# Kernel tuning notes

Hardware: AMD Instinct MI355X
Metric: run time of the kernel (lower is better)

Reference implementation:

```python
import jax, jax.numpy as jnp
import numpy as np
from jax import lax

BLANK = 27
NEG = -1e30  # safe -inf substitute (avoids NaN grads through logaddexp)


def _joint_log_probs(enc, dec, We, Wd, bf, Wp, bp):
    # Concat-then-Linear == sum of per-branch matmuls: [e;d] @ Wf = e@We + d@Wd.
    f = jnp.einsum('bte,eh->bth', enc, We)          # [B,T,H]
    g = jnp.einsum('bud,dh->buh', dec, Wd)          # [B,U1,H]
    h = jnp.tanh(f[:, :, None, :] + g[:, None, :, :] + bf)  # [B,T,U1,H]
    logits = jnp.einsum('btuh,hv->btuv', h, Wp) + bp         # [B,T,U1,V]
    return jax.nn.log_softmax(logits, axis=-1)


def _rnnt_loss_one(lp, tgt, t_len, u_len):
    # lp: [T,U1,V] log-probs, tgt: [U] int labels, t_len/u_len: scalars.
    T, U1, V = lp.shape
    blank_lp = lp[:, :, BLANK]                                   # [T,U1]
    lab_lp = jnp.take_along_axis(lp[:, :U1 - 1, :],
                                 tgt[None, :, None], axis=2)[..., 0]  # [T,U]

    # alpha[0,:] : only label emissions along u at t=0.
    alpha0 = jnp.concatenate([jnp.zeros((1,), lp.dtype),
                              jnp.cumsum(lab_lp[0])])            # [U1]

    def step(prev_alpha, inp):
        b_prev, lab_t = inp                       # [U1], [U]
        from_below = prev_alpha + b_prev          # blank move from t-1
        first = from_below[0]

        def inner(carry, x):
            fb, lab = x
            new = jnp.logaddexp(fb, carry + lab)  # blank-from-below vs label-from-left
            return new, new

        _, rest = lax.scan(inner, first, (from_below[1:], lab_t))
        alpha_t = jnp.concatenate([first[None], rest])
        return alpha_t, alpha_t

    _, alphas = lax.scan(step, alpha0, (blank_lp[:-1], lab_lp[1:]))
    alpha = jnp.concatenate([alpha0[None], alphas], axis=0)      # [T,U1]

    # Terminal: emit final blank at (t_len-1, u_len).
    return -(alpha[t_len - 1, u_len] + blank_lp[t_len - 1, u_len])


def setup_inputs() -> dict:
    key = jax.random.key(0)
    ks = jax.random.split(key, 10)
    B, T, U, E, D, H, V = 8, 400, 60, 256, 256, 512, 28
    enc_state = jax.random.normal(ks[0], (B, T, E), jnp.float32)
    dec_state = jax.random.normal(ks[1], (B, U + 1, D), jnp.float32)
    targets = jax.random.randint(ks[2], (B, U), 0, BLANK, jnp.int32)
    inputs_length = jax.random.randint(ks[3], (B,), 200, T + 1, jnp.int32)
    targets_length = jax.random.randint(ks[4], (B,), 30, U + 1, jnp.int32)
    s1 = 1.0 / np.sqrt(E + D)
    s2 = 1.0 / np.sqrt(H)
    We = jax.random.normal(ks[5], (E, H), jnp.float32) * s1
    Wd = jax.random.normal(ks[6], (D, H), jnp.float32) * s1
    bf = jax.random.normal(ks[7], (H,), jnp.float32) * s1
    Wp = jax.random.normal(ks[8], (H, V), jnp.float32) * s2
    bp = jax.random.normal(ks[9], (V,), jnp.float32) * s2
    return {"enc_state": enc_state, "dec_state": dec_state,
            "We": We, "Wd": Wd, "bf": bf, "Wp": Wp, "bp": bp,
            "targets": targets, "inputs_length": inputs_length,
            "targets_length": targets_length}


def reference(enc_state, dec_state, We, Wd, bf, Wp, bp,
              targets, inputs_length, targets_length):
    lp = _joint_log_probs(enc_state, dec_state, We, Wd, bf, Wp, bp)
    loss = jax.vmap(_rnnt_loss_one)(lp, targets, inputs_length, targets_length)
    return loss  # [B], reduction='none'
```

## Files before the change

kernel.cpp:

```cpp
#include <hip/hip_runtime.h>
#include <hip/hip_bf16.h>
#include <math.h>

#define NEGF (-1e30f)
#define LOG2E 1.4426950408889634f
#define LN2F 0.6931471805599453f
#define TSCALE 2.885390081777927f

typedef __attribute__((ext_vector_type(8))) short bf16x8;
typedef __attribute__((ext_vector_type(4))) float f32x4;

#define DROWS_PAD 480
#define DPITCH 64
#define CH 48

__device__ __forceinline__ unsigned short f2bf(float x) {
    __hip_bfloat16 h = __float2bfloat16(x);
    return *reinterpret_cast<unsigned short*>(&h);
}

__device__ __forceinline__ float wave_shr1(float x) {
    int i = __builtin_bit_cast(int, x);
    int r = __builtin_amdgcn_update_dpp(0, i, 0x138, 0xf, 0xf, true);
    return __builtin_bit_cast(float, r);
}

__device__ __forceinline__ float4 rcp4_nr(float4 d) {
    float4 y;
    y.x = __builtin_bit_cast(float, 0x7EF311C3 - __builtin_bit_cast(int, d.x));
    y.y = __builtin_bit_cast(float, 0x7EF311C3 - __builtin_bit_cast(int, d.y));
    y.z = __builtin_bit_cast(float, 0x7EF311C3 - __builtin_bit_cast(int, d.z));
    y.w = __builtin_bit_cast(float, 0x7EF311C3 - __builtin_bit_cast(int, d.w));
    float4 t;
    t.x = fmaf(-d.x, y.x, 2.f); t.y = fmaf(-d.y, y.y, 2.f);
    t.z = fmaf(-d.z, y.z, 2.f); t.w = fmaf(-d.w, y.w, 2.f);
    y.x *= t.x; y.y *= t.y; y.z *= t.z; y.w *= t.w;
    return y;
}

__global__ __launch_bounds__(256) void k_pack(const float* __restrict__ We,
                                              const float* __restrict__ Wd,
                                              const float* __restrict__ Wp,
                                              const float* __restrict__ bp,
                                              unsigned short* __restrict__ WeFrag,
                                              unsigned short* __restrict__ WdFrag,
                                              unsigned short* __restrict__ BfragP,
                                              float* __restrict__ csbp) {
    int gid = blockIdx.x * 256 + threadIdx.x;
    if (gid < 32768) {
        const float* W = (gid < 16384) ? We : Wd;
        unsigned short* F = (gid < 16384) ? WeFrag : WdFrag;
        int s = gid & 16383;
        int lane = s & 63;
        int c = (s >> 6) & 7;
        int nt = s >> 9;
        int n = nt * 16 + (lane & 15);
        int kbase = c * 32 + ((lane >> 4) & 3) * 8;
        unsigned short* dst = F + (size_t)s * 8;
#pragma unroll
        for (int j = 0; j < 8; ++j) dst[j] = f2bf(W[(size_t)(kbase + j) * 512 + n]);
    } else if (gid < 34816) {
        int s = gid - 32768;
        int lane = s & 63;
        int half = (s >> 6) & 1;
        int c = s >> 7;
        int n = half * 16 + (lane & 15);
        int kbase = c * 32 + (lane >> 4) * 8;
        unsigned short* dst = BfragP + (size_t)s * 8;
#pragma unroll
        for (int j = 0; j < 8; ++j) {
            float v = (n < 28) ? (-2.f * Wp[(kbase + j) * 28 + n]) : 0.f;
            dst[j] = f2bf(v);
        }
    } else if (gid < 34848) {
        int v = gid - 34816;
        float s = 0.f;
        if (v < 28) {
            for (int k = 0; k < 512; ++k) s += Wp[k * 28 + v];
            s += bp[v];
        }
        csbp[v] = s;
    }
}

__global__ __launch_bounds__(256) void k_gemm(const float* __restrict__ enc,
                                              const float* __restrict__ dec,
                                              const float* __restrict__ bfv,
                                              const unsigned short* __restrict__ WeFrag,
                                              const unsigned short* __restrict__ WdFrag,
                                              float* __restrict__ f,
                                              float* __restrict__ g) {
    const int wid = blockIdx.x * 4 + threadIdx.y;
    const int lane = threadIdx.x;
    const int m16 = lane & 15;
    const int quad = lane >> 4;

    const float* A; const unsigned short* WF; float* Out; int M, rt, ct; bool isg;
    if (wid < 1600) { A = enc; WF = WeFrag; Out = f; M = 3200; rt = wid >> 3; ct = wid & 7; isg = false; }
    else { int w2 = wid - 1600; A = dec; WF = WdFrag; Out = g; M = 488; rt = w2 >> 3; ct = w2 & 7; isg = true; }

    const int row = rt * 16 + m16;
    const float* arow = A + (size_t)min(row, M - 1) * 256 + quad * 8;

    f32x4 acc[4];
#pragma unroll
    for (int i = 0; i < 4; ++i) acc[i] = (f32x4){0.f, 0.f, 0.f, 0.f};

#pragma unroll
    for (int c = 0; c < 8; ++c) {
        float4 a0 = *(const float4*)(arow + c * 32);
        float4 a1 = *(const float4*)(arow + c * 32 + 4);
        union { unsigned short s[8]; bf16x8 v; } Af;
        Af.s[0] = f2bf(a0.x); Af.s[1] = f2bf(a0.y);
        Af.s[2] = f2bf(a0.z); Af.s[3] = f2bf(a0.w);
        Af.s[4] = f2bf(a1.x); Af.s[5] = f2bf(a1.y);
        Af.s[6] = f2bf(a1.z); Af.s[7] = f2bf(a1.w);
#pragma unroll
        for (int i = 0; i < 4; ++i) {
            int nt = ct * 4 + i;
            bf16x8 Bv = *(const bf16x8*)(WF + (size_t)((nt * 8 + c) * 64 + lane) * 8);
            acc[i] = __builtin_amdgcn_mfma_f32_16x16x32_bf16(Af.v, Bv, acc[i], 0, 0, 0);
        }
    }

#pragma unroll
    for (int i = 0; i < 4; ++i) {
        int n = ct * 64 + i * 16 + m16;
        float bv = isg ? bfv[n] : 0.f;
#pragma unroll
        for (int r = 0; r < 4; ++r) {
            int ro = rt * 16 + quad * 4 + r;
            if (ro < M) Out[(size_t)ro * 512 + n] = (acc[i][r] + bv) * TSCALE;
        }
    }
}

__global__ __launch_bounds__(512, 4) void k_cells(const float* __restrict__ f,
                                                  const float* __restrict__ g,
                                                  const unsigned short* __restrict__ Bfrag,
                                                  const float* __restrict__ csbp,
                                                  const int* __restrict__ targets,
                                                  const int* __restrict__ ilen,
                                                  const int* __restrict__ ulenp,
                                                  float2* __restrict__ pairD) {
    const int b = blockIdx.z;
    const int tlen = ilen[b];
    const int ulen = ulenp[b];
    const int t0 = blockIdx.x * 16;
    if (t0 >= tlen) return;
    if ((int)blockIdx.y * 8 > ulen) return;
    const int wave = threadIdx.y;
    const int lane = threadIdx.x;
    const int tid = wave * 64 + lane;

    __shared__ float fs[16 * 516];

    {
        const float4* src = (const float4*)(f + (size_t)(b * 400 + t0) * 512);
#pragma unroll
        for (int i = 0; i < 4; ++i) {
            int idx = tid + i * 512;
            int row = idx >> 7;
            int c4 = idx & 127;
            float4 v = src[idx];
            *(float4*)&fs[row * 516 + c4 * 4] = v;
        }
    }
    __syncthreads();

    const int quad = lane >> 4;
    const int m16 = lane & 15;
    const int u_raw = blockIdx.y * 8 + wave;
    const int u = min(u_raw, 60);
    const float* fsrow = fs + m16 * 516 + quad * 8;
    const float* gu = g + (size_t)(b * 61 + u) * 512 + quad * 8;
    const float4 one4 = make_float4(1.f, 1.f, 1.f, 1.f);

    f32x4 acc0 = {0.f, 0.f, 0.f, 0.f};
    f32x4 acc1 = {0.f, 0.f, 0.f, 0.f};

    float4 FA[2], FB[2], GA[2], GB[2];
    bf16x8 BR0[2], BR1[2];
#pragma unroll
    for (int c0 = 0; c0 < 2; ++c0) {
        FA[c0] = *(const float4*)(fsrow + c0 * 32);
        FB[c0] = *(const float4*)(fsrow + c0 * 32 + 4);
        GA[c0] = *(const float4*)(gu + c0 * 32);
        GB[c0] = *(const float4*)(gu + c0 * 32 + 4);
        BR0[c0] = *(const bf16x8*)(Bfrag + ((size_t)((c0 * 2 + 0) * 64 + lane)) * 8);
        BR1[c0] = *(const bf16x8*)(Bfrag + ((size_t)((c0 * 2 + 1) * 64 + lane)) * 8);
    }

#pragma unroll
    for (int c = 0; c < 16; ++c) {
        const int cu = c & 1;
        float4 fa = FA[cu], fb = FB[cu], ga = GA[cu], gb = GB[cu];
        bf16x8 b0 = BR0[cu], b1 = BR1[cu];
        if (c < 14) {
            FA[cu] = *(const float4*)(fsrow + (c + 2) * 32);
            FB[cu] = *(const float4*)(fsrow + (c + 2) * 32 + 4);
            GA[cu] = *(const float4*)(gu + (c + 2) * 32);
            GB[cu] = *(const float4*)(gu + (c + 2) * 32 + 4);
            BR0[cu] = *(const bf16x8*)(Bfrag + ((size_t)(((c + 2) * 2 + 0) * 64 + lane)) * 8);
            BR1[cu] = *(const bf16x8*)(Bfrag + ((size_t)(((c + 2) * 2 + 1) * 64 + lane)) * 8);
        }
        float4 s0 = fa + ga;
        float4 s1 = fb + gb;
        float4 e0, e1;
        e0.x = __builtin_amdgcn_exp2f(s0.x); e0.y = __builtin_amdgcn_exp2f(s0.y);
        e0.z = __builtin_amdgcn_exp2f(s0.z); e0.w = __builtin_amdgcn_exp2f(s0.w);
        e1.x = __builtin_amdgcn_exp2f(s1.x); e1.y = __builtin_amdgcn_exp2f(s1.y);
        e1.z = __builtin_amdgcn_exp2f(s1.z); e1.w = __builtin_amdgcn_exp2f(s1.w);
        float4 r0 = rcp4_nr(e0 + one4);
        float4 r1 = rcp4_nr(e1 + one4);
        union { unsigned short s[8]; bf16x8 v; } A;
        A.s[0] = f2bf(r0.x); A.s[1] = f2bf(r0.y);
        A.s[2] = f2bf(r0.z); A.s[3] = f2bf(r0.w);
        A.s[4] = f2bf(r1.x); A.s[5] = f2bf(r1.y);
        A.s[6] = f2bf(r1.z); A.s[7] = f2bf(r1.w);
        acc0 = __builtin_amdgcn_mfma_f32_16x16x32_bf16(A.v, b0, acc0, 0, 0, 0);
        acc1 = __builtin_amdgcn_mfma_f32_16x16x32_bf16(A.v, b1, acc1, 0, 0, 0);
    }

    const float cs0 = csbp[m16];
    const int n1 = 16 + m16;
    const bool n1v = (n1 < 28);
    const float cs1 = csbp[n1 & 31];
    int tv = targets[b * 60 + min(u, 59)];

    float res_blank[4], res_lab[4];
#pragma unroll
    for (int r = 0; r < 4; ++r) {
        float l0 = acc0[r] + cs0;
        float l1 = n1v ? (acc1[r] + cs1) : NEGF;
        float mx = fmaxf(l0, l1);
        mx = fmaxf(mx, __shfl_xor(mx, 1, 64));
        mx = fmaxf(mx, __shfl_xor(mx, 2, 64));
        mx = fmaxf(mx, __shfl_xor(mx, 4, 64));
        mx = fmaxf(mx, __shfl_xor(mx, 8, 64));
        float s = __builtin_amdgcn_exp2f((l0 - mx) * LOG2E) +
                  __builtin_amdgcn_exp2f((l1 - mx) * LOG2E);
        s += __shfl_xor(s, 1, 64);
        s += __shfl_xor(s, 2, 64);
        s += __shfl_xor(s, 4, 64);
        s += __shfl_xor(s, 8, 64);
        float lse = mx + __logf(s);
        int base = lane & 48;
        float labsrc = (tv < 16) ? l0 : l1;
        float labv = __shfl(labsrc, base | (tv & 15), 64);
        float blankv = __shfl(l1, base | 11, 64);
        res_blank[r] = (blankv - lse) * LOG2E;
        res_lab[r] = (labv - lse) * LOG2E;
    }

    if (m16 == 0 && u_raw <= 60) {
        float2* Pd = pairD + (size_t)b * (DROWS_PAD * DPITCH);
#pragma unroll
        for (int r = 0; r < 4; ++r) {
            int t = t0 + quad * 4 + r;
            if (t < tlen) {
                int d = t + u;
                float2 pr;
                pr.x = res_blank[r];
                pr.y = (u <= 59) ? res_lab[r] : NEGF;
                Pd[d * DPITCH + u] = pr;
            }
        }
    }
}

__global__ __launch_bounds__(256) void k_alpha(const float2* __restrict__ pairD,
                                               const int* __restrict__ ilen,
                                               const int* __restrict__ ulenp,
                                               float* __restrict__ out) {
    const int b = blockIdx.x;
    const int u = threadIdx.x;
    const int w = threadIdx.y;
    const float2* Pd = pairD + (size_t)b * (DROWS_PAD * DPITCH);
    const int tl = ilen[b];
    const int ul = ulenp[b];
    const int dstar = tl - 1 + ul;
    const int NCH = (dstar + CH - 1) / CH;
    const bool uok = (u <= 60);
    const bool lok = (u >= 1 && u <= 60);

    __shared__ char lbuf[2 * CH * 512];

    {
        const int tid = w * 64 + u;
        const float4* gs = (const float4*)Pd;
        float4* ld = (float4*)lbuf;
#pragma unroll
        for (int j = 0; j < 6; ++j) ld[tid + j * 256] = gs[tid + j * 256];
    }
    __syncthreads();

    float cur = (u == 0) ? 0.f : NEGF;
    float saved = NEGF, savedBlank = NEGF;

    for (int k = 0; k < NCH; ++k) {
        if (w > 0 && (k + 1) < NCH) {
            const int pt = (w - 1) * 64 + u;
            const float4* gs = (const float4*)(Pd + (size_t)(k + 1) * CH * DPITCH);
            float4* ld = (float4*)(lbuf + ((k + 1) & 1) * (CH * 512));
#pragma unroll
            for (int j = 0; j < 8; ++j)
                ld[pt + j * 192] = gs[pt + j * 192];
        }
        if (w == 0) {
            const char* base = lbuf + (k & 1) * (CH * 512);
            const int d0 = k * CH + 1;
#pragma unroll 16
            for (int r = 0; r < CH; ++r) {
                const int d = d0 + r;
                float2 v = *(const float2*)(base + r * 512 + u * 8);
                int t = d - u;
                float bv = (t >= 1 && t <= 399 && uok) ? v.x : NEGF;
                float lvn = wave_shr1(v.y);
                float lv = (lok && t >= 0 && t <= 399) ? lvn : NEGF;
                float up = wave_shr1(cur);
                float a = cur + bv;
                float c2 = up + lv;
                float mx = fmaxf(a, c2), mn = fminf(a, c2);
                float nv = mx + __log2f(1.f + __builtin_amdgcn_exp2f(mn - mx));
                bool valid = (t >= 0 && t <= 399 && uok);
                cur = valid ? nv : cur;
                saved = (d == dstar) ? cur : saved;
                savedBlank = (d == dstar) ? v.x : savedBlank;
            }
        }
        __syncthreads();
    }
    if (w == 0 && u == ul) out[b] = -(saved + savedBlank) * LN2F;
}

extern "C" void kernel_launch(void* const* d_in, const int* in_sizes, int n_in,
                              void* d_out, int out_size, void* d_ws, size_t ws_size,
                              hipStream_t stream) {
    const float* enc = (const float*)d_in[0];
    const float* dec = (const float*)d_in[1];
    const float* We  = (const float*)d_in[2];
    const float* Wd  = (const float*)d_in[3];
    const float* bf  = (const float*)d_in[4];
    const float* Wp  = (const float*)d_in[5];
    const float* bp  = (const float*)d_in[6];
    const int* targets = (const int*)d_in[7];
    const int* ilen    = (const int*)d_in[8];
    const int* ulen    = (const int*)d_in[9];
    float* out = (float*)d_out;
    float* ws = (float*)d_ws;

    float* f     = ws;
    float* g     = ws + 1638400;
    unsigned short* BfragP = (unsigned short*)(ws + 1888256);
    unsigned short* WeFrag = (unsigned short*)(ws + 1896448);
    unsigned short* WdFrag = (unsigned short*)(ws + 1961984);
    float* csbp  = ws + 2027520;
    float2* pairD = (float2*)(ws + 2027552);

    k_pack<<<137, 256, 0, stream>>>(We, Wd, Wp, bp, WeFrag, WdFrag, BfragP, csbp);

    k_gemm<<<462, dim3(64, 4, 1), 0, stream>>>(enc, dec, bf, WeFrag, WdFrag, f, g);

    dim3 gridC(25, 8, 8);
    dim3 blockC(64, 8, 1);
    k_cells<<<gridC, blockC, 0, stream>>>(f, g, BfragP, csbp, targets, ilen, ulen, pairD);

    k_alpha<<<8, dim3(64, 4, 1), 0, stream>>>(pairD, ilen, ulen, out);
}
```

Measured before the change: 142.9 us.

## Fuse alpha recursion into cells kernel with per-chunk completion counters

Removes the separate alpha launch and runs the alpha recursion in eight extra blocks of the cells kernel, one per batch element. These blocks poll per-(batch, time-chunk) atomic counters that cell blocks bump when they finish, and start each diagonal chunk once the time chunks it needs are done. The aim is to overlap the serial alpha scan with cell production and to drop one kernel launch boundary. The cost is spinning blocks that hold CU slots, relaxed atomic stores and loads with no explicit fences, and a counter reset added to the pack kernel.

```diff
diff --git a/kernel.cpp b/kernel.cpp
--- a/kernel.cpp
+++ b/kernel.cpp
@@ -45,7 +45,8 @@
                                               unsigned short* __restrict__ WeFrag,
                                               unsigned short* __restrict__ WdFrag,
                                               unsigned short* __restrict__ BfragP,
-                                              float* __restrict__ csbp) {
+                                              float* __restrict__ csbp,
+                                              int* __restrict__ doneCnt) {
     int gid = blockIdx.x * 256 + threadIdx.x;
     if (gid < 32768) {
         const float* W = (gid < 16384) ? We : Wd;
@@ -80,6 +81,8 @@
             s += bp[v];
         }
         csbp[v] = s;
+    } else if (gid < 35104) {
+        doneCnt[gid - 34848] = 0;
     }
 }
 
@@ -142,7 +145,95 @@
                                                   const int* __restrict__ targets,
                                                   const int* __restrict__ ilen,
                                                   const int* __restrict__ ulenp,
-                                                  float2* __restrict__ pairD) {
+                                                  float2* __restrict__ pairD,
+                                                  int* __restrict__ doneCnt,
+                                                  float* __restrict__ out) {
+    __shared__ char smem[49152];
+
+    if (blockIdx.x == 25) {
+        if (blockIdx.z != 0) return;
+        const int w = threadIdx.y;
+        if (w >= 4) return;
+        const int b = blockIdx.y;
+        const int u = threadIdx.x;
+        const float2* Pd = pairD + (size_t)b * (DROWS_PAD * DPITCH);
+        const unsigned long long* Pq = (const unsigned long long*)Pd;
+        const int* dn = doneCnt + b * 32;
+        const int tl = ilen[b];
+        const int ul = ulenp[b];
+        const int dstar = tl - 1 + ul;
+        const int NCH = (dstar + CH - 1) / CH;
+        const int tcLast = (tl - 1) >> 4;
+        const int nU = (ul >> 3) + 1;
+        const bool uok = (u <= 60);
+        const bool lok = (u >= 1 && u <= 60);
+        unsigned long long* lq = (unsigned long long*)smem;
+
+        int tcCur = -1;
+        auto gate = [&](int need) {
+            need = min(need, tcLast);
+            int guard = 0;
+            while (tcCur < need) {
+                int c_ = __hip_atomic_load(dn + tcCur + 1, __ATOMIC_RELAXED,
+                                           __HIP_MEMORY_SCOPE_AGENT);
+                if (c_ >= nU) { ++tcCur; }
+                else { __builtin_amdgcn_s_sleep(2);
+                       if (++guard > (1 << 22)) break; }
+            }
+        };
+
+        gate(2);
+        {
+            const int tid = w * 64 + u;
+#pragma unroll
+            for (int j = 0; j < 12; ++j)
+                lq[tid + j * 256] = __hip_atomic_load(Pq + tid + j * 256,
+                                        __ATOMIC_RELAXED, __HIP_MEMORY_SCOPE_AGENT);
+        }
+        __syncthreads();
+
+        float cur = (u == 0) ? 0.f : NEGF;
+        float saved = NEGF, savedBlank = NEGF;
+
+        for (int k = 0; k < NCH; ++k) {
+            if (w > 0 && (k + 1) < NCH) {
+                gate(3 * (k + 1) + 2);
+                const int pt = (w - 1) * 64 + u;
+                const unsigned long long* gs = Pq + (size_t)(k + 1) * (CH * DPITCH);
+                unsigned long long* ld = lq + ((k + 1) & 1) * (CH * 64);
+#pragma unroll
+                for (int j = 0; j < 16; ++j)
+                    ld[pt + j * 192] = __hip_atomic_load(gs + pt + j * 192,
+                                           __ATOMIC_RELAXED, __HIP_MEMORY_SCOPE_AGENT);
+            }
+            if (w == 0) {
+                const unsigned long long* baseq = lq + (k & 1) * (CH * 64);
+                const int d0 = k * CH + 1;
+#pragma unroll 16
+                for (int r = 0; r < CH; ++r) {
+                    const int d = d0 + r;
+                    float2 v = __builtin_bit_cast(float2, baseq[r * 64 + u]);
+                    int t = d - u;
+                    float bv = (t >= 1 && t <= 399 && uok) ? v.x : NEGF;
+                    float lvn = wave_shr1(v.y);
+                    float lv = (lok && t >= 0 && t <= 399) ? lvn : NEGF;
+                    float up = wave_shr1(cur);
+                    float a = cur + bv;
+                    float c2 = up + lv;
+                    float mx = fmaxf(a, c2), mn = fminf(a, c2);
+                    float nv = mx + __log2f(1.f + __builtin_amdgcn_exp2f(mn - mx));
+                    bool valid = (t >= 0 && t <= 399 && uok);
+                    cur = valid ? nv : cur;
+                    saved = (d == dstar) ? cur : saved;
+                    savedBlank = (d == dstar) ? v.x : savedBlank;
+                }
+            }
+            __syncthreads();
+        }
+        if (w == 0 && u == ul) out[b] = -(saved + savedBlank) * LN2F;
+        return;
+    }
+
     const int b = blockIdx.z;
     const int tlen = ilen[b];
     const int ulen = ulenp[b];
@@ -152,8 +243,7 @@
     const int wave = threadIdx.y;
     const int lane = threadIdx.x;
     const int tid = wave * 64 + lane;
-
-    __shared__ float fs[16 * 516];
+    float* fs = (float*)smem;
 
     {
         const float4* src = (const float4*)(f + (size_t)(b * 400 + t0) * 512);
@@ -263,75 +353,18 @@
                 float2 pr;
                 pr.x = res_blank[r];
                 pr.y = (u <= 59) ? res_lab[r] : NEGF;
-                Pd[d * DPITCH + u] = pr;
+                __hip_atomic_store((unsigned long long*)&Pd[d * DPITCH + u],
+                                   __builtin_bit_cast(unsigned long long, pr),
+                                   __ATOMIC_RELAXED, __HIP_MEMORY_SCOPE_AGENT);
             }
         }
     }
-}
-
-__global__ __launch_bounds__(256) void k_alpha(const float2* __restrict__ pairD,
-                                               const int* __restrict__ ilen,
-                                               const int* __restrict__ ulenp,
-                                               float* __restrict__ out) {
-    const int b = blockIdx.x;
-    const int u = threadIdx.x;
-    const int w = threadIdx.y;
-    const float2* Pd = pairD + (size_t)b * (DROWS_PAD * DPITCH);
-    const int tl = ilen[b];
-    const int ul = ulenp[b];
-    const int dstar = tl - 1 + ul;
-    const int NCH = (dstar + CH - 1) / CH;
-    const bool uok = (u <= 60);
-    const bool lok = (u >= 1 && u <= 60);
-
-    __shared__ char lbuf[2 * CH * 512];
-
-    {
-        const int tid = w * 64 + u;
-        const float4* gs = (const float4*)Pd;
-        float4* ld = (float4*)lbuf;
-#pragma unroll
-        for (int j = 0; j < 6; ++j) ld[tid + j * 256] = gs[tid + j * 256];
-    }
+
     __syncthreads();
-
-    float cur = (u == 0) ? 0.f : NEGF;
-    float saved = NEGF, savedBlank = NEGF;
-
-    for (int k = 0; k < NCH; ++k) {
-        if (w > 0 && (k + 1) < NCH) {
-            const int pt = (w - 1) * 64 + u;
-            const float4* gs = (const float4*)(Pd + (size_t)(k + 1) * CH * DPITCH);
-            float4* ld = (float4*)(lbuf + ((k + 1) & 1) * (CH * 512));
-#pragma unroll
-            for (int j = 0; j < 8; ++j)
-                ld[pt + j * 192] = gs[pt + j * 192];
-        }
-        if (w == 0) {
-            const char* base = lbuf + (k & 1) * (CH * 512);
-            const int d0 = k * CH + 1;
-#pragma unroll 16
-            for (int r = 0; r < CH; ++r) {
-                const int d = d0 + r;
-                float2 v = *(const float2*)(base + r * 512 + u * 8);
-                int t = d - u;
-                float bv = (t >= 1 && t <= 399 && uok) ? v.x : NEGF;
-                float lvn = wave_shr1(v.y);
-                float lv = (lok && t >= 0 && t <= 399) ? lvn : NEGF;
-                float up = wave_shr1(cur);
-                float a = cur + bv;
-                float c2 = up + lv;
-                float mx = fmaxf(a, c2), mn = fminf(a, c2);
-                float nv = mx + __log2f(1.f + __builtin_amdgcn_exp2f(mn - mx));
-                bool valid = (t >= 0 && t <= 399 && uok);
-                cur = valid ? nv : cur;
-                saved = (d == dstar) ? cur : saved;
-                savedBlank = (d == dstar) ? v.x : savedBlank;
-            }
-        }
-        __syncthreads();
-    }
-    if (w == 0 && u == ul) out[b] = -(saved + savedBlank) * LN2F;
+    if (tid == 0) {
+        __hip_atomic_fetch_add(doneCnt + b * 32 + blockIdx.x, 1,
+                               __ATOMIC_RELAXED, __HIP_MEMORY_SCOPE_AGENT);
+    }
 }
 
 extern "C" void kernel_launch(void* const* d_in, const int* in_sizes, int n_in,
@@ -357,14 +390,14 @@
     unsigned short* WdFrag = (unsigned short*)(ws + 1961984);
     float* csbp  = ws + 2027520;
     float2* pairD = (float2*)(ws + 2027552);
-
-    k_pack<<<137, 256, 0, stream>>>(We, Wd, Wp, bp, WeFrag, WdFrag, BfragP, csbp);
+    int* doneCnt = (int*)(ws + 2519072);
+
+    k_pack<<<138, 256, 0, stream>>>(We, Wd, Wp, bp, WeFrag, WdFrag, BfragP, csbp, doneCnt);
 
     k_gemm<<<462, dim3(64, 4, 1), 0, stream>>>(enc, dec, bf, WeFrag, WdFrag, f, g);
 
-    dim3 gridC(25, 8, 8);
+    dim3 gridC(26, 8, 8);
     dim3 blockC(64, 8, 1);
-    k_cells<<<gridC, blockC, 0, stream>>>(f, g, BfragP, csbp, targets, ilen, ulen, pairD);
-
-    k_alpha<<<8, dim3(64, 4, 1), 0, stream>>>(pairD, ilen, ulen, out);
-}
+    k_cells<<<gridC, blockC, 0, stream>>>(f, g, BfragP, csbp, targets, ilen, ulen,
+                                          pairD, doneCnt, out);
+}
```

Result: slower. 158.9 us (+11.2%).
